# Kernel tuning notes

Hardware: AMD Instinct MI355X
Metric: run time of the kernel (lower is better)

The kernel has to match this reference:

```python
import jax, jax.numpy as jnp
import numpy as np

N, E = 50000, 800000
F_IN, HID, HEADS, NCLS = 128, 64, 4, 16
NEG_SLOPE = 0.2


def setup_inputs() -> dict:
    key = jax.random.key(0)
    ks = jax.random.split(key, 16)
    def glorot(k, shape):
        fan_in, fan_out = shape[0], shape[-1]
        lim = jnp.sqrt(6.0 / (fan_in + fan_out))
        return jax.random.uniform(k, shape, jnp.float32, -lim, lim)
    x = jax.random.normal(ks[0], (N, F_IN), jnp.float32)
    edge_index = jax.random.randint(ks[1], (2, E), 0, N, dtype=jnp.int64)
    inp = {"x": x, "edge_index": edge_index}
    # layer 1: F_IN -> HID x HEADS (concat)
    inp["W1"] = glorot(ks[2], (F_IN, HEADS * HID))
    inp["a1_src"] = glorot(ks[3], (HEADS, HID))
    inp["a1_dst"] = glorot(ks[4], (HEADS, HID))
    inp["b1"] = jnp.zeros((HEADS * HID,), jnp.float32)
    # layer 2: HEADS*HID -> HID x HEADS (concat)
    inp["W2"] = glorot(ks[5], (HEADS * HID, HEADS * HID))
    inp["a2_src"] = glorot(ks[6], (HEADS, HID))
    inp["a2_dst"] = glorot(ks[7], (HEADS, HID))
    inp["b2"] = jnp.zeros((HEADS * HID,), jnp.float32)
    # layer 3: HEADS*HID -> NCLS, heads=1, concat=False (mean)
    inp["W3"] = glorot(ks[8], (HEADS * HID, NCLS))
    inp["a3_src"] = glorot(ks[9], (1, NCLS))
    inp["a3_dst"] = glorot(ks[10], (1, NCLS))
    inp["b3"] = jnp.zeros((NCLS,), jnp.float32)
    return inp


def gat_conv(x, src, dst, W, a_src, a_dst, b, heads, out_dim, concat):
    n = x.shape[0]
    h = (x @ W).reshape(n, heads, out_dim)           # [N, H, D]
    s_src = jnp.sum(h * a_src, axis=-1)              # [N, H]
    s_dst = jnp.sum(h * a_dst, axis=-1)              # [N, H]
    e = jax.nn.leaky_relu(s_src[src] + s_dst[dst], NEG_SLOPE)  # [E, H]
    # segment softmax over incoming edges of each dst node
    m = jax.ops.segment_max(e, dst, num_segments=n)
    ex = jnp.exp(e - m[dst])
    z = jax.ops.segment_sum(ex, dst, num_segments=n)
    alpha = ex / z[dst]                              # [E, H]
    msg = h[src] * alpha[:, :, None]                 # [E, H, D]
    out = jax.ops.segment_sum(msg, dst, num_segments=n)  # [N, H, D]
    out = out.reshape(n, heads * out_dim) if concat else out.mean(axis=1)
    return out + b


def reference(x, edge_index, W1, a1_src, a1_dst, b1, W2, a2_src, a2_dst, b2,
              W3, a3_src, a3_dst, b3):
    n = x.shape[0]
    loop = jnp.arange(n, dtype=edge_index.dtype)
    src = jnp.concatenate([edge_index[0], loop])     # add self-loops (PyG default)
    dst = jnp.concatenate([edge_index[1], loop])
    h = jax.nn.elu(gat_conv(x, src, dst, W1, a1_src, a1_dst, b1, HEADS, HID, True))
    h = jax.nn.elu(gat_conv(h, src, dst, W2, a2_src, a2_dst, b2, HEADS, HID, True))
    h = gat_conv(h, src, dst, W3, a3_src, a3_dst, b3, 1, NCLS, False)
    return jax.nn.log_softmax(h, axis=1)
```

## Files before the change

kernel.cpp:

```cpp
#include <hip/hip_runtime.h>
#include <hip/hip_bf16.h>
#include <math.h>

#define N_NODES 50000
#define N_EDGES 800000
#define F_IN    128
#define HID     64
#define HEADS   4
#define NCLS    16
#define NEG_SLOPE 0.2f

typedef __attribute__((ext_vector_type(8))) _Float16 half8v;
typedef __attribute__((ext_vector_type(4))) float f32x4;
typedef __attribute__((ext_vector_type(2))) float f32x2;

static __device__ __forceinline__ float lrelu(float x) {
    return x >= 0.f ? x : NEG_SLOPE * x;
}
static __device__ __forceinline__ unsigned short f2h(float f) {
    _Float16 h = (_Float16)f;
    return __builtin_bit_cast(unsigned short, h);
}
static __device__ __forceinline__ float h2f(unsigned short u) {
    return (float)__builtin_bit_cast(_Float16, u);
}

__global__ void k_zero(int4* __restrict__ p, int n4) {
    int i = blockIdx.x * blockDim.x + threadIdx.x;
    if (i < n4) p[i] = int4{0, 0, 0, 0};
}

#define NB_WT1  128
#define NB_WT2  256
#define NB_WT3  16
#define NB_HIST 3125
__global__ void k_prep(const float* __restrict__ W1, unsigned short* __restrict__ W1t,
                       const float* __restrict__ W2, unsigned short* __restrict__ W2t,
                       const float* __restrict__ W3, unsigned short* __restrict__ W3ht,
                       const int* __restrict__ dst, int* __restrict__ counts,
                       unsigned short* __restrict__ rank) {
    int bid = blockIdx.x, tid = threadIdx.x;
    if (bid < NB_WT1) {
        int i = bid * 256 + tid;
        int k = i >> 8, c = i & 255;
        W1t[c * F_IN + k] = f2h(W1[i]);
    } else if (bid < NB_WT1 + NB_WT2) {
        int i = (bid - NB_WT1) * 256 + tid;
        int k = i >> 8, c = i & 255;
        W2t[c * 256 + k] = f2h(W2[i]);
    } else if (bid < NB_WT1 + NB_WT2 + NB_WT3) {
        int i = (bid - NB_WT1 - NB_WT2) * 256 + tid;
        int k = i >> 4, c = i & 15;
        W3ht[c * 256 + k] = f2h(W3[i]);
    } else {
        int i = (bid - NB_WT1 - NB_WT2 - NB_WT3) * 256 + tid;
        if (i < N_EDGES) rank[i] = (unsigned short)atomicAdd(&counts[dst[i]], 1);
    }
}

__global__ __launch_bounds__(256) void k_scan1(const int* __restrict__ counts, int* __restrict__ incl,
                                               int* __restrict__ bsums, int n) {
    __shared__ int wsum[4];
    int blk = blockIdx.x, tid = threadIdx.x;
    int lane = tid & 63, w = tid >> 6;
    int i0 = blk * 1024 + tid * 4;
    int v[4];
    #pragma unroll
    for (int j = 0; j < 4; j++) v[j] = (i0 + j < n) ? counts[i0 + j] : 0;
    int t = v[0] + v[1] + v[2] + v[3];
    int x = t;
    #pragma unroll
    for (int d = 1; d < 64; d <<= 1) { int y = __shfl_up(x, d); if (lane >= d) x += y; }
    if (lane == 63) wsum[w] = x;
    __syncthreads();
    int woff = 0;
    #pragma unroll
    for (int ww = 0; ww < 4; ww++) woff += (ww < w) ? wsum[ww] : 0;
    int p = woff + x - t;
    #pragma unroll
    for (int j = 0; j < 4; j++) { p += v[j]; if (i0 + j < n) incl[i0 + j] = p; }
    if (tid == 255) bsums[blk] = woff + x;
}

__global__ void k_scan2(const int* __restrict__ bsums, int* __restrict__ boffs, int nb, int* rowptr_end) {
    int lane = threadIdx.x;
    int v = (lane < nb) ? bsums[lane] : 0;
    int x = v;
    #pragma unroll
    for (int d = 1; d < 64; d <<= 1) { int y = __shfl_up(x, d); if (lane >= d) x += y; }
    if (lane < nb) boffs[lane] = x - v;
    if (lane == 63) *rowptr_end = x;
}

__global__ void k_scan3(const int* __restrict__ incl, const int* __restrict__ counts,
                        const int* __restrict__ boffs, int* __restrict__ rowptr, int n) {
    int i = blockIdx.x * blockDim.x + threadIdx.x;
    if (i < n) rowptr[i] = boffs[i >> 10] + incl[i] - counts[i];
}

static __device__ __forceinline__ int swz(int r, int lc) {
    return r * 4 + (lc ^ (r & 3) ^ ((r >> 2) & 1));
}

template<int CONVA>
static __device__ __forceinline__ void gemm_body(
        int bid, const void* __restrict__ Av, const unsigned short* __restrict__ Bt,
        const float* __restrict__ asrc, const float* __restrict__ adst,
        unsigned char* __restrict__ C8, float* __restrict__ s_src, float* __restrict__ s_dst,
        int M, int K, unsigned short* Asm, unsigned short* Bsm) {
    int tid = threadIdx.x;
    int lane = tid & 63, wid = tid >> 6;
    int bx = bid & 1, by = bid >> 1;
    int row0 = by * 128, col0 = bx * 128;
    int wr = wid >> 1, wc = wid & 1;
    f32x4 acc[4][4] = {};

    for (int k0 = 0; k0 < K; k0 += 32) {
        __syncthreads();
        #pragma unroll
        for (int s = 0; s < 2; s++) {
            int c = tid + s * 256;
            int row = c >> 2, lc = c & 3;
            int gr = row0 + row; if (gr >= M) gr = 0;
            uint4 va;
            if (CONVA) {
                const float* Af = (const float*)Av + (size_t)gr * K + k0 + lc * 8;
                float4 fa = *(const float4*)Af;
                float4 fb = *(const float4*)(Af + 4);
                va.x = (unsigned)f2h(fa.x) | ((unsigned)f2h(fa.y) << 16);
                va.y = (unsigned)f2h(fa.z) | ((unsigned)f2h(fa.w) << 16);
                va.z = (unsigned)f2h(fb.x) | ((unsigned)f2h(fb.y) << 16);
                va.w = (unsigned)f2h(fb.z) | ((unsigned)f2h(fb.w) << 16);
            } else {
                va = *(const uint4*)((const unsigned short*)Av + (size_t)gr * K + k0 + lc * 8);
            }
            *(uint4*)(&Asm[swz(row, lc) * 8]) = va;
            uint4 vb = *(const uint4*)(Bt + (size_t)(col0 + row) * K + k0 + lc * 8);
            *(uint4*)(&Bsm[swz(row, lc) * 8]) = vb;
        }
        __syncthreads();
        half8v af[4], bg[4];
        int lq = lane >> 4;
        #pragma unroll
        for (int m = 0; m < 4; m++) {
            int r = wr * 64 + m * 16 + (lane & 15);
            af[m] = *(const half8v*)(&Asm[swz(r, lq) * 8]);
        }
        #pragma unroll
        for (int n = 0; n < 4; n++) {
            int r = wc * 64 + n * 16 + (lane & 15);
            bg[n] = *(const half8v*)(&Bsm[swz(r, lq) * 8]);
        }
        #pragma unroll
        for (int m = 0; m < 4; m++)
            #pragma unroll
            for (int n = 0; n < 4; n++)
                acc[m][n] = __builtin_amdgcn_mfma_f32_16x16x32_f16(af[m], bg[n], acc[m][n], 0, 0, 0);
    }

    #pragma unroll
    for (int m = 0; m < 4; m++) {
        #pragma unroll
        for (int r = 0; r < 4; r++) {
            int row = row0 + wr * 64 + m * 16 + (lane >> 4) * 4 + r;
            if (row < M) {
                int q01 = __builtin_amdgcn_cvt_pk_fp8_f32(acc[m][0][r], acc[m][1][r], 0, false);
                int q23 = __builtin_amdgcn_cvt_pk_fp8_f32(acc[m][2][r], acc[m][3][r], 0, false);
                size_t base = (size_t)row * 256 + col0 + wc * 64 + (lane & 15);
                C8[base]      = (unsigned char)(q01 & 0xff);
                C8[base + 16] = (unsigned char)((q01 >> 8) & 0xff);
                C8[base + 32] = (unsigned char)(q23 & 0xff);
                C8[base + 48] = (unsigned char)((q23 >> 8) & 0xff);
            }
        }
    }

    int c16 = lane & 15, lq = lane >> 4;
    int head = bx * 2 + wc;
    float avs[4], avd[4];
    #pragma unroll
    for (int nn = 0; nn < 4; nn++) {
        avs[nn] = asrc[head * 64 + nn * 16 + c16];
        avd[nn] = adst[head * 64 + nn * 16 + c16];
    }
    #pragma unroll
    for (int mm = 0; mm < 4; mm++) {
        #pragma unroll
        for (int r = 0; r < 4; r++) {
            float ps = 0.f, pd = 0.f;
            #pragma unroll
            for (int nn = 0; nn < 4; nn++) {
                ps += acc[mm][nn][r] * avs[nn];
                pd += acc[mm][nn][r] * avd[nn];
            }
            #pragma unroll
            for (int off = 1; off < 16; off <<= 1) {
                ps += __shfl_xor(ps, off);
                pd += __shfl_xor(pd, off);
            }
            if (c16 == 0) {
                int grow = row0 + wr * 64 + mm * 16 + lq * 4 + r;
                if (grow < M) {
                    s_src[grow * 4 + head] = ps;
                    s_dst[grow * 4 + head] = pd;
                }
            }
        }
    }
}

__global__ __launch_bounds__(256) void k_gemm_mfma(const unsigned short* __restrict__ A,
                                                   const unsigned short* __restrict__ Bt,
                                                   const float* __restrict__ asrc,
                                                   const float* __restrict__ adst,
                                                   unsigned char* __restrict__ C8,
                                                   float* __restrict__ s_src,
                                                   float* __restrict__ s_dst,
                                                   int M, int K) {
    __shared__ unsigned short Asm[128 * 32];
    __shared__ unsigned short Bsm[128 * 32];
    gemm_body<0>(blockIdx.x, A, Bt, asrc, adst, C8, s_src, s_dst, M, K, Asm, Bsm);
}

__global__ __launch_bounds__(256) void k_b(const float* __restrict__ A,
                                           const unsigned short* __restrict__ Bt,
                                           const float* __restrict__ asrc,
                                           const float* __restrict__ adst,
                                           unsigned char* __restrict__ C8,
                                           float* __restrict__ s_src,
                                           float* __restrict__ s_dst,
                                           int M, int K, int gemmBlocks,
                                           const int* __restrict__ src, const int* __restrict__ dst,
                                           const int* __restrict__ rowptr,
                                           const unsigned short* __restrict__ rank,
                                           unsigned short* __restrict__ col, int e) {
    __shared__ unsigned short Asm[128 * 32];
    __shared__ unsigned short Bsm[128 * 32];
    int bid = blockIdx.x;
    if (bid < gemmBlocks) {
        gemm_body<1>(bid, A, Bt, asrc, adst, C8, s_src, s_dst, M, K, Asm, Bsm);
    } else {
        int half = (e + 1) >> 1;
        int i = (bid - gemmBlocks) * 256 + (int)threadIdx.x;
        if (i < half) {
            int d = dst[i];
            col[rowptr[d] + rank[i]] = (unsigned short)src[i];
        }
        int j = i + half;
        if (j < e) {
            int d = dst[j];
            col[rowptr[d] + rank[j]] = (unsigned short)src[j];
        }
    }
}

#define PEDGE(SV, SD) __expf(fminf(lrelu((SV) + (SD)), 80.f))
#define ACC8(P, HV) { \
    f32x2 pbc = {(P), (P)}; \
    f32x2 v0 = __builtin_amdgcn_cvt_pk_f32_fp8((HV).x, false); \
    f32x2 v1 = __builtin_amdgcn_cvt_pk_f32_fp8((HV).x, true);  \
    f32x2 v2 = __builtin_amdgcn_cvt_pk_f32_fp8((HV).y, false); \
    f32x2 v3 = __builtin_amdgcn_cvt_pk_f32_fp8((HV).y, true);  \
    asm("v_pk_fma_f32 %0, %1, %2, %0" : "+v"(a01) : "v"(v0), "v"(pbc)); \
    asm("v_pk_fma_f32 %0, %1, %2, %0" : "+v"(a23) : "v"(v1), "v"(pbc)); \
    asm("v_pk_fma_f32 %0, %1, %2, %0" : "+v"(a45) : "v"(v2), "v"(pbc)); \
    asm("v_pk_fma_f32 %0, %1, %2, %0" : "+v"(a67) : "v"(v3), "v"(pbc)); \
    z += (P); }

static __device__ __forceinline__ uint4 agg_core(
        int node, int n, int head, int j8, int base8, unsigned foff,
        const unsigned char* __restrict__ h8, const int* __restrict__ rowptr,
        const unsigned short* __restrict__ col,
        const float* __restrict__ s_src, const float* __restrict__ s_dst,
        const float* __restrict__ bias, int l5) {
    uint4 ov = {0, 0, 0, 0};
    if (node >= n) return ov;
    int rs = rowptr[node], re = rowptr[node + 1];
    float sd = s_dst[node * 4 + head];
    float z = 0.f;
    f32x2 a01 = {0.f, 0.f}, a23 = {0.f, 0.f}, a45 = {0.f, 0.f}, a67 = {0.f, 0.f};
    {
        float pself = PEDGE(s_src[node * 4 + head], sd);
        uint2 own = *(const uint2*)(h8 + (((unsigned)node << 8) + foff));
        ACC8(pself, own);
    }
    int i = rs;
    for (; i + 7 < re; i += 8) {
        unsigned cc[8];
        #pragma unroll
        for (int j = 0; j < 8; j++) cc[j] = col[i + j];
        float s_own = s_src[cc[j8] * 4 + head];
        uint2 hv[8];
        #pragma unroll
        for (int j = 0; j < 8; j++)
            hv[j] = *(const uint2*)(h8 + ((cc[j] << 8) + foff));
        float p_own = PEDGE(s_own, sd);
        float pv[8];
        #pragma unroll
        for (int j = 0; j < 8; j++) pv[j] = __shfl(p_own, base8 + j);
        #pragma unroll
        for (int j = 0; j < 8; j++) { ACC8(pv[j], hv[j]); }
    }
    for (; i + 3 < re; i += 4) {
        unsigned cc[4];
        #pragma unroll
        for (int j = 0; j < 4; j++) cc[j] = col[i + j];
        float s_own = s_src[cc[j8 & 3] * 4 + head];
        uint2 hv[4];
        #pragma unroll
        for (int j = 0; j < 4; j++)
            hv[j] = *(const uint2*)(h8 + ((cc[j] << 8) + foff));
        float p_own = PEDGE(s_own, sd);
        float pv[4];
        #pragma unroll
        for (int j = 0; j < 4; j++) pv[j] = __shfl(p_own, base8 + j);
        #pragma unroll
        for (int j = 0; j < 4; j++) { ACC8(pv[j], hv[j]); }
    }
    for (; i < re; i++) {
        unsigned c0 = col[i];
        float s0 = s_src[c0 * 4 + head];
        uint2 h0 = *(const uint2*)(h8 + ((c0 << 8) + foff));
        float p0 = PEDGE(s0, sd);
        ACC8(p0, h0);
    }
    float inv = 1.f / z;
    int f0 = l5 * 8;
    float4 bv0 = *(const float4*)(bias + f0);
    float4 bv1 = *(const float4*)(bias + f0 + 4);
    float o[8];
    o[0] = a01.x * inv + bv0.x; o[1] = a01.y * inv + bv0.y;
    o[2] = a23.x * inv + bv0.z; o[3] = a23.y * inv + bv0.w;
    o[4] = a45.x * inv + bv1.x; o[5] = a45.y * inv + bv1.y;
    o[6] = a67.x * inv + bv1.z; o[7] = a67.y * inv + bv1.w;
    #pragma unroll
    for (int j = 0; j < 8; j++) o[j] = o[j] > 0.f ? o[j] : __expf(o[j]) - 1.f;
    unsigned* wd = (unsigned*)&ov;
    #pragma unroll
    for (int j = 0; j < 4; j++)
        wd[j] = (unsigned)f2h(o[2 * j]) | ((unsigned)f2h(o[2 * j + 1]) << 16);
    return ov;
}

__global__ void k_aggregate(const unsigned char* __restrict__ h8, const int* __restrict__ rowptr,
                            const unsigned short* __restrict__ col,
                            const float* __restrict__ s_src, const float* __restrict__ s_dst,
                            const float* __restrict__ bias,
                            unsigned short* __restrict__ out, int n) {
    int wave = (blockIdx.x * blockDim.x + threadIdx.x) >> 6;
    int lane = threadIdx.x & 63;
    int half = lane >> 5, l5 = lane & 31;
    int node = wave * 2 + half;
    if (node >= n) return;
    int head = l5 >> 3;
    int j8 = l5 & 7;
    int base8 = lane & ~7;
    unsigned foff = (unsigned)(l5 * 8);
    uint4 ov = agg_core(node, n, head, j8, base8, foff, h8, rowptr, col, s_src, s_dst, bias, l5);
    *(uint4*)(out + (size_t)node * 256 + l5 * 8) = ov;
}

__global__ __launch_bounds__(256) void k_agg2(
        const unsigned char* __restrict__ h8, const int* __restrict__ rowptr,
        const unsigned short* __restrict__ col,
        const float* __restrict__ s_src, const float* __restrict__ s_dst,
        const float* __restrict__ bias,
        const unsigned short* __restrict__ W3ht,
        const float* __restrict__ a3s, const float* __restrict__ a3d,
        unsigned short* __restrict__ h3,
        float* __restrict__ s_src3, float* __restrict__ s_dst3, int n) {
    __shared__ unsigned short ALds[16 * 264];
    int tid = threadIdx.x;
    int lane = tid & 63, wv = tid >> 6;
    int half = lane >> 5, l5 = lane & 31;
    int nl = wv * 2 + half;
    int node = blockIdx.x * 8 + nl;
    for (int i = tid; i < (8 * 264) / 2; i += 256) ((unsigned*)&ALds[8 * 264])[i] = 0;

    int head = l5 >> 3;
    int j8 = l5 & 7;
    int base8 = lane & ~7;
    unsigned foff = (unsigned)(l5 * 8);
    uint4 ov = agg_core(node, n, head, j8, base8, foff, h8, rowptr, col, s_src, s_dst, bias, l5);
    *(uint4*)(&ALds[nl * 264 + l5 * 8]) = ov;
    __syncthreads();

    if (wv == 0) {
        int col16 = lane & 15, lq = lane >> 4;
        f32x4 acc3 = {0.f, 0.f, 0.f, 0.f};
        #pragma unroll
        for (int ks = 0; ks < 8; ks++) {
            half8v af = *(const half8v*)(&ALds[col16 * 264 + ks * 32 + lq * 8]);
            half8v bg = *(const half8v*)(W3ht + col16 * 256 + ks * 32 + lq * 8);
            acc3 = __builtin_amdgcn_mfma_f32_16x16x32_f16(af, bg, acc3, 0, 0, 0);
        }
        float a3sv = a3s[col16], a3dv = a3d[col16];
        #pragma unroll
        for (int r = 0; r < 4; r++) {
            int row = lq * 4 + r;
            int gnode = blockIdx.x * 8 + row;
            float v = acc3[r];
            float ps = v * a3sv, pd = v * a3dv;
            #pragma unroll
            for (int off = 1; off < 16; off <<= 1) {
                ps += __shfl_xor(ps, off);
                pd += __shfl_xor(pd, off);
            }
            if (row < 8 && gnode < n) {
                h3[(size_t)gnode * 16 + col16] = f2h(v);
                if (col16 == 0) { s_src3[gnode] = ps; s_dst3[gnode] = pd; }
            }
        }
    }
}

__global__ void k_agg3(const unsigned short* __restrict__ h3, const int* __restrict__ rowptr,
                       const unsigned short* __restrict__ col,
                       const float* __restrict__ s_src, const float* __restrict__ s_dst,
                       const float* __restrict__ b3,
                       float* __restrict__ outp, int n) {
    int wave = (blockIdx.x * blockDim.x + threadIdx.x) >> 6;
    int lane = threadIdx.x & 63;
    if (wave >= n) return;
    int g = lane >> 4, c = lane & 15;
    int gbase = lane & ~15;
    int rs = rowptr[wave], re = rowptr[wave + 1];
    float sdn = s_dst[wave];

    float z = 0.f, acc = 0.f;
    if (g == 0) {
        float p = __expf(fminf(lrelu(s_src[wave] + sdn), 80.f));
        z += p;
        acc += p * h2f(h3[(size_t)wave * 16 + c]);
    }
    int i = rs + g;
    for (; i + 12 < re; i += 16) {
        int ss[4];
        #pragma unroll
        for (int j = 0; j < 4; j++) ss[j] = col[i + 4 * j];
        float q_own = s_src[ss[c & 3]];
        float v0 = h2f(h3[(size_t)ss[0] * 16 + c]), v1 = h2f(h3[(size_t)ss[1] * 16 + c]);
        float v2 = h2f(h3[(size_t)ss[2] * 16 + c]), v3 = h2f(h3[(size_t)ss[3] * 16 + c]);
        float p_own = __expf(fminf(lrelu(q_own + sdn), 80.f));
        float p0 = __shfl(p_own, gbase + 0);
        float p1 = __shfl(p_own, gbase + 1);
        float p2 = __shfl(p_own, gbase + 2);
        float p3 = __shfl(p_own, gbase + 3);
        z += (p0 + p1) + (p2 + p3);
        acc += p0 * v0 + p1 * v1 + p2 * v2 + p3 * v3;
    }
    for (; i < re; i += 4) {
        int s = col[i];
        float p = __expf(fminf(lrelu(s_src[s] + sdn), 80.f));
        z += p;
        acc += p * h2f(h3[(size_t)s * 16 + c]);
    }
    z += __shfl_xor(z, 16);  z += __shfl_xor(z, 32);
    acc += __shfl_xor(acc, 16); acc += __shfl_xor(acc, 32);
    if (lane < 16) {
        float v = acc / z + b3[c];
        float mm = v;
        #pragma unroll
        for (int off = 1; off < 16; off <<= 1) mm = fmaxf(mm, __shfl_xor(mm, off));
        float se = __expf(v - mm);
        #pragma unroll
        for (int off = 1; off < 16; off <<= 1) se += __shfl_xor(se, off);
        outp[(size_t)wave * 16 + c] = v - mm - logf(se);
    }
}

extern "C" void kernel_launch(void* const* d_in, const int* in_sizes, int n_in,
                              void* d_out, int out_size, void* d_ws, size_t ws_size,
                              hipStream_t stream) {
    const float* x      = (const float*)d_in[0];
    const int*   ei     = (const int*)d_in[1];
    const float* W1     = (const float*)d_in[2];
    const float* a1_src = (const float*)d_in[3];
    const float* a1_dst = (const float*)d_in[4];
    const float* b1     = (const float*)d_in[5];
    const float* W2     = (const float*)d_in[6];
    const float* a2_src = (const float*)d_in[7];
    const float* a2_dst = (const float*)d_in[8];
    const float* b2     = (const float*)d_in[9];
    const float* W3     = (const float*)d_in[10];
    const float* a3_src = (const float*)d_in[11];
    const float* a3_dst = (const float*)d_in[12];
    const float* b3     = (const float*)d_in[13];
    float* outp = (float*)d_out;

    const int N = N_NODES, E = N_EDGES;
    const int* src = ei;
    const int* dst = ei + E;

    char* ws = (char*)d_ws;
    size_t off = 0;
    auto alloc = [&](size_t bytes) {
        void* p = ws + off;
        off = (off + bytes + 255) & ~(size_t)255;
        return p;
    };
    int*   rowptr = (int*)alloc((N + 1) * sizeof(int));
    int*   counts = (int*)alloc(N * sizeof(int));
    unsigned short* col = (unsigned short*)alloc(E * sizeof(short));
    unsigned short* rank = (unsigned short*)alloc(E * sizeof(short));
    int*   incl   = (int*)alloc(N * sizeof(int));
    int*   bsums  = (int*)alloc(64 * sizeof(int));
    int*   boffs  = (int*)alloc(64 * sizeof(int));
    float* s_src  = (float*)alloc((size_t)N * HEADS * sizeof(float));
    float* s_dst  = (float*)alloc((size_t)N * HEADS * sizeof(float));
    float* s_src3 = (float*)alloc((size_t)N * sizeof(float));
    float* s_dst3 = (float*)alloc((size_t)N * sizeof(float));
    unsigned short* W1t = (unsigned short*)alloc((size_t)256 * F_IN * sizeof(short));
    unsigned short* W2t = (unsigned short*)alloc((size_t)256 * 256 * sizeof(short));
    unsigned short* W3ht = (unsigned short*)alloc((size_t)16 * 256 * sizeof(short));
    unsigned char* hA8  = (unsigned char*)alloc((size_t)N * 256);
    unsigned short* hB  = (unsigned short*)alloc((size_t)N * 256 * sizeof(short));
    unsigned short* h3  = (unsigned short*)alloc((size_t)N * 16 * sizeof(short));
    (void)ws_size;

    const int aggBlocks  = (N + 3) / 4;
    const int aggBlocks2 = (N + 7) / 8;
    const int gemmBlocks = ((N + 127) / 128) * 2;
    const int scatBlocks = ((E + 1) / 2 + 255) / 256;

    k_zero<<<(N / 4 + 255) / 256, 256, 0, stream>>>((int4*)counts, N / 4);
    k_prep<<<NB_WT1 + NB_WT2 + NB_WT3 + NB_HIST, 256, 0, stream>>>(W1, W1t, W2, W2t, W3, W3ht,
                                                                   dst, counts, rank);

    const int nb = (N + 1023) / 1024;
    k_scan1<<<nb, 256, 0, stream>>>(counts, incl, bsums, N);
    k_scan2<<<1, 64, 0, stream>>>(bsums, boffs, nb, rowptr + N);
    k_scan3<<<(N + 255) / 256, 256, 0, stream>>>(incl, counts, boffs, rowptr, N);

    k_b<<<gemmBlocks + scatBlocks, 256, 0, stream>>>(x, W1t, a1_src, a1_dst, hA8, s_src, s_dst,
                                                     N, F_IN, gemmBlocks,
                                                     src, dst, rowptr, rank, col, E);
    k_aggregate<<<aggBlocks2, 256, 0, stream>>>(hA8, rowptr, col, s_src, s_dst, b1, hB, N);
    k_gemm_mfma<<<gemmBlocks, 256, 0, stream>>>(hB, W2t, a2_src, a2_dst, hA8, s_src, s_dst, N, 256);
    k_agg2<<<aggBlocks2, 256, 0, stream>>>(hA8, rowptr, col, s_src, s_dst, b2,
                                           W3ht, a3_src, a3_dst, h3, s_src3, s_dst3, N);
    k_agg3<<<aggBlocks, 256, 0, stream>>>(h3, rowptr, col, s_src3, s_dst3, b3, outp, N);
}
```

Baseline: 204.5 us.

## Fuse layer-1 aggregation with layer-2 GEMM into one kernel

Replaces the separate layer-1 aggregate kernel and layer-2 MFMA GEMM with one kernel. Each block aggregates 16 nodes into shared memory as fp16, then multiplies that tile by W2 using MFMA. It writes fp8 features and the attention scores directly. This removes the fp16 hB round trip through global memory and one launch. In exchange, W2 is read from global or L2 per 16-row block with no LDS reuse, and separate buffers are needed to avoid overwriting inputs.

```diff
diff --git a/kernel.cpp b/kernel.cpp
--- a/kernel.cpp
+++ b/kernel.cpp
@@ -209,19 +209,6 @@
     }
 }
 
-__global__ __launch_bounds__(256) void k_gemm_mfma(const unsigned short* __restrict__ A,
-                                                   const unsigned short* __restrict__ Bt,
-                                                   const float* __restrict__ asrc,
-                                                   const float* __restrict__ adst,
-                                                   unsigned char* __restrict__ C8,
-                                                   float* __restrict__ s_src,
-                                                   float* __restrict__ s_dst,
-                                                   int M, int K) {
-    __shared__ unsigned short Asm[128 * 32];
-    __shared__ unsigned short Bsm[128 * 32];
-    gemm_body<0>(blockIdx.x, A, Bt, asrc, adst, C8, s_src, s_dst, M, K, Asm, Bsm);
-}
-
 __global__ __launch_bounds__(256) void k_b(const float* __restrict__ A,
                                            const unsigned short* __restrict__ Bt,
                                            const float* __restrict__ asrc,
@@ -342,22 +329,86 @@
     return ov;
 }
 
-__global__ void k_aggregate(const unsigned char* __restrict__ h8, const int* __restrict__ rowptr,
-                            const unsigned short* __restrict__ col,
-                            const float* __restrict__ s_src, const float* __restrict__ s_dst,
-                            const float* __restrict__ bias,
-                            unsigned short* __restrict__ out, int n) {
-    int wave = (blockIdx.x * blockDim.x + threadIdx.x) >> 6;
-    int lane = threadIdx.x & 63;
+__global__ __launch_bounds__(256) void k_fuse2(
+        const unsigned char* __restrict__ h8, const int* __restrict__ rowptr,
+        const unsigned short* __restrict__ col,
+        const float* __restrict__ s_src, const float* __restrict__ s_dst,
+        const float* __restrict__ bias,
+        const unsigned short* __restrict__ W2t,
+        const float* __restrict__ a2s, const float* __restrict__ a2d,
+        unsigned char* __restrict__ C8,
+        float* __restrict__ s_src2, float* __restrict__ s_dst2, int n) {
+    __shared__ unsigned short ALds[16 * 264];
+    int tid = threadIdx.x;
+    int lane = tid & 63, wv = tid >> 6;
     int half = lane >> 5, l5 = lane & 31;
-    int node = wave * 2 + half;
-    if (node >= n) return;
-    int head = l5 >> 3;
-    int j8 = l5 & 7;
-    int base8 = lane & ~7;
+    int head = l5 >> 3, j8 = l5 & 7, base8 = lane & ~7;
     unsigned foff = (unsigned)(l5 * 8);
-    uint4 ov = agg_core(node, n, head, j8, base8, foff, h8, rowptr, col, s_src, s_dst, bias, l5);
-    *(uint4*)(out + (size_t)node * 256 + l5 * 8) = ov;
+
+    #pragma unroll
+    for (int p = 0; p < 2; p++) {
+        int nl = wv * 4 + p * 2 + half;
+        int node = blockIdx.x * 16 + nl;
+        uint4 ov = agg_core(node, n, head, j8, base8, foff, h8, rowptr, col,
+                            s_src, s_dst, bias, l5);
+        *(uint4*)(&ALds[nl * 264 + l5 * 8]) = ov;
+    }
+    __syncthreads();
+
+    int c16 = lane & 15, lq = lane >> 4;
+    int cw = wv * 64;
+    f32x4 acc[4] = {};
+    #pragma unroll
+    for (int ks = 0; ks < 8; ks++) {
+        half8v af = *(const half8v*)(&ALds[c16 * 264 + ks * 32 + lq * 8]);
+        #pragma unroll
+        for (int nn = 0; nn < 4; nn++) {
+            half8v bg = *(const half8v*)(W2t + (size_t)(cw + nn * 16 + c16) * 256 + ks * 32 + lq * 8);
+            acc[nn] = __builtin_amdgcn_mfma_f32_16x16x32_f16(af, bg, acc[nn], 0, 0, 0);
+        }
+    }
+    #pragma unroll
+    for (int r = 0; r < 4; r++) {
+        int row = blockIdx.x * 16 + lq * 4 + r;
+        if (row < n) {
+            int q01 = __builtin_amdgcn_cvt_pk_fp8_f32(acc[0][r], acc[1][r], 0, false);
+            int q23 = __builtin_amdgcn_cvt_pk_fp8_f32(acc[2][r], acc[3][r], 0, false);
+            size_t base = (size_t)row * 256 + cw + c16;
+            C8[base]      = (unsigned char)(q01 & 0xff);
+            C8[base + 16] = (unsigned char)((q01 >> 8) & 0xff);
+            C8[base + 32] = (unsigned char)(q23 & 0xff);
+            C8[base + 48] = (unsigned char)((q23 >> 8) & 0xff);
+        }
+    }
+    {
+        float avs[4], avd[4];
+        #pragma unroll
+        for (int nn = 0; nn < 4; nn++) {
+            avs[nn] = a2s[wv * 64 + nn * 16 + c16];
+            avd[nn] = a2d[wv * 64 + nn * 16 + c16];
+        }
+        #pragma unroll
+        for (int r = 0; r < 4; r++) {
+            float ps = 0.f, pd = 0.f;
+            #pragma unroll
+            for (int nn = 0; nn < 4; nn++) {
+                ps += acc[nn][r] * avs[nn];
+                pd += acc[nn][r] * avd[nn];
+            }
+            #pragma unroll
+            for (int off = 1; off < 16; off <<= 1) {
+                ps += __shfl_xor(ps, off);
+                pd += __shfl_xor(pd, off);
+            }
+            if (c16 == 0) {
+                int gnode = blockIdx.x * 16 + lq * 4 + r;
+                if (gnode < n) {
+                    s_src2[gnode * 4 + wv] = ps;
+                    s_dst2[gnode * 4 + wv] = pd;
+                }
+            }
+        }
+    }
 }
 
 __global__ __launch_bounds__(256) void k_agg2(
@@ -508,18 +559,21 @@
     int*   boffs  = (int*)alloc(64 * sizeof(int));
     float* s_src  = (float*)alloc((size_t)N * HEADS * sizeof(float));
     float* s_dst  = (float*)alloc((size_t)N * HEADS * sizeof(float));
+    float* s_src2 = (float*)alloc((size_t)N * HEADS * sizeof(float));
+    float* s_dst2 = (float*)alloc((size_t)N * HEADS * sizeof(float));
     float* s_src3 = (float*)alloc((size_t)N * sizeof(float));
     float* s_dst3 = (float*)alloc((size_t)N * sizeof(float));
     unsigned short* W1t = (unsigned short*)alloc((size_t)256 * F_IN * sizeof(short));
     unsigned short* W2t = (unsigned short*)alloc((size_t)256 * 256 * sizeof(short));
     unsigned short* W3ht = (unsigned short*)alloc((size_t)16 * 256 * sizeof(short));
     unsigned char* hA8  = (unsigned char*)alloc((size_t)N * 256);
-    unsigned short* hB  = (unsigned short*)alloc((size_t)N * 256 * sizeof(short));
+    unsigned char* hB8  = (unsigned char*)alloc((size_t)N * 256);
     unsigned short* h3  = (unsigned short*)alloc((size_t)N * 16 * sizeof(short));
     (void)ws_size;
 
     const int aggBlocks  = (N + 3) / 4;
-    const int aggBlocks2 = (N + 7) / 8;
+    const int agg2Blocks = (N + 7) / 8;
+    const int fuseBlocks = (N + 15) / 16;
     const int gemmBlocks = ((N + 127) / 128) * 2;
     const int scatBlocks = ((E + 1) / 2 + 255) / 256;
 
@@ -535,9 +589,9 @@
     k_b<<<gemmBlocks + scatBlocks, 256, 0, stream>>>(x, W1t, a1_src, a1_dst, hA8, s_src, s_dst,
                                                      N, F_IN, gemmBlocks,
                                                      src, dst, rowptr, rank, col, E);
-    k_aggregate<<<aggBlocks2, 256, 0, stream>>>(hA8, rowptr, col, s_src, s_dst, b1, hB, N);
-    k_gemm_mfma<<<gemmBlocks, 256, 0, stream>>>(hB, W2t, a2_src, a2_dst, hA8, s_src, s_dst, N, 256);
-    k_agg2<<<aggBlocks2, 256, 0, stream>>>(hA8, rowptr, col, s_src, s_dst, b2,
+    k_fuse2<<<fuseBlocks, 256, 0, stream>>>(hA8, rowptr, col, s_src, s_dst, b1,
+                                            W2t, a2_src, a2_dst, hB8, s_src2, s_dst2, N);
+    k_agg2<<<agg2Blocks, 256, 0, stream>>>(hB8, rowptr, col, s_src2, s_dst2, b2,
                                            W3ht, a3_src, a3_dst, h3, s_src3, s_dst3, N);
     k_agg3<<<aggBlocks, 256, 0, stream>>>(h3, rowptr, col, s_src3, s_dst3, b3, outp, N);
 }
```

Result: slower. 241.7 us (+18.2%).
